# Kernel optimization log

Measured on AMD Instinct MI355X. Metric: run time of the kernel, lower is better.

## Reference

```python
import jax, jax.numpy as jnp
import numpy as np

TOKENS, IN_F, OUT_F = 65536, 1024, 1024


def setup_inputs() -> dict:
    key = jax.random.key(0)
    kx, kw = jax.random.split(key)
    x = jax.random.normal(kx, (TOKENS, IN_F), dtype=jnp.float32)
    weight = jax.random.normal(kw, (OUT_F, IN_F), dtype=jnp.float32) * 0.05
    return {"x": x, "weight": weight}


def reference(x, weight):
    # per-output-row scale: alpha = mean(|w|) over in_features
    alpha = jnp.mean(jnp.abs(weight), axis=1, keepdims=True)  # [out, 1]
    w_bin = jnp.sign(weight) * alpha                          # [out, in]
    # F.linear(x, w_bin) == x @ w_bin.T
    return jnp.einsum("ti,oi->to", x, w_bin)
```

## Files before the change

### kernel.cpp

```cpp
#include <hip/hip_runtime.h>


typedef _Float16 half8 __attribute__((ext_vector_type(8)));
typedef _Float16 half4v __attribute__((ext_vector_type(4)));
typedef float f32x4 __attribute__((ext_vector_type(4)));

#define TOKENS 65536
#define INF 1024
#define OUTF 1024
#define BM 256
#define BN 256
#define BK 32
#define NKT 32

__device__ __forceinline__ void gload_lds16(const void* g, void* l) {
  __builtin_amdgcn_global_load_lds(
      (const __attribute__((address_space(1))) unsigned int*)g,
      (__attribute__((address_space(3))) unsigned int*)l, 16, 0, 0);
}

__device__ __forceinline__ half8 cvt8(f32x4 a, f32x4 b) {
  half8 h;
  h[0] = (_Float16)a[0]; h[1] = (_Float16)a[1];
  h[2] = (_Float16)a[2]; h[3] = (_Float16)a[3];
  h[4] = (_Float16)b[0]; h[5] = (_Float16)b[1];
  h[6] = (_Float16)b[2]; h[7] = (_Float16)b[3];
  return h;
}

#define ALOAD(d0, d1, ap)                                                      \
  asm volatile("global_load_dwordx4 %0, %2, off\n\t"                           \
               "global_load_dwordx4 %1, %2, off offset:16"                     \
               : "=&v"(d0), "=&v"(d1)                                          \
               : "v"(ap)                                                       \
               : "memory")

__global__ __launch_bounds__(256) void bl_prep(const float* __restrict__ w,
                                               _Float16* __restrict__ sbin,
                                               float* __restrict__ alpha) {
  const int o = blockIdx.x;
  const int tid = threadIdx.x;
  const float4 v = ((const float4*)(w + (size_t)o * INF))[tid];
  float s = fabsf(v.x) + fabsf(v.y) + fabsf(v.z) + fabsf(v.w);
  half4v h;
  h[0] = (_Float16)((v.x > 0.f) ? 1.f : ((v.x < 0.f) ? -1.f : 0.f));
  h[1] = (_Float16)((v.y > 0.f) ? 1.f : ((v.y < 0.f) ? -1.f : 0.f));
  h[2] = (_Float16)((v.z > 0.f) ? 1.f : ((v.z < 0.f) ? -1.f : 0.f));
  h[3] = (_Float16)((v.w > 0.f) ? 1.f : ((v.w < 0.f) ? -1.f : 0.f));
  *(half4v*)(sbin + (size_t)o * INF + tid * 4) = h;
#pragma unroll
  for (int off = 32; off > 0; off >>= 1) s += __shfl_down(s, off, 64);
  __shared__ float red[4];
  const int wave = tid >> 6, lane = tid & 63;
  if (lane == 0) red[wave] = s;
  __syncthreads();
  if (tid == 0) alpha[o] = (red[0] + red[1] + red[2] + red[3]) * (1.0f / 1024.0f);
}

__global__ __launch_bounds__(512, 1) void bl_gemm(const float* __restrict__ x,
                                                  const _Float16* __restrict__ sbin,
                                                  const float* __restrict__ alpha,
                                                  float* __restrict__ out) {
  __shared__ _Float16 ldsA[4][BM * BK];
  __shared__ _Float16 ldsB[4][BN * BK];

  const int tid = threadIdx.x;
  const int lane = tid & 63;
  const int wid = tid >> 6;
  const int l15 = lane & 15;
  const int kc = lane >> 4;
  const int wr = wid >> 2;
  const int wc = wid & 3;

  const int bid = blockIdx.x;
  const int wgid = (bid & 7) * 128 + (bid >> 3);
  const int bm0 = (wgid >> 2) * BM;
  const int bn0 = (wgid & 3) * BN;

  const int rw = tid >> 2;
  const int cA = tid & 3;
  const int swz = cA ^ ((rw >> 1) & 3);

  size_t aOff[2], bOff[2];
  int aWr[2], bDst[2];
#pragma unroll
  for (int h = 0; h < 2; ++h) {
    aOff[h] = (size_t)(bm0 + h * 128 + rw) * INF + cA * 8;
    bOff[h] = (size_t)(bn0 + h * 128 + rw) * INF + swz * 8;
    aWr[h] = (h * 128 + rw) * 64 + swz * 16;
    bDst[h] = h * 8192 + tid * 16;
  }
  const int sl = (kc ^ ((l15 >> 1) & 3)) * 16;
  const int aRdB = (wr * 128 + l15) * 64 + sl;
  const int bRdB = (wc * 64 + l15) * 64 + sl;

  f32x4 acc[8][4] = {};
  f32x4 stA[2][2][2];
  half8 bf0, bf1, bf2, bf3;

  {
#pragma unroll
    for (int t = 0; t < 2; ++t)
#pragma unroll
      for (int h = 0; h < 2; ++h) {
        f32x4 v0 = *(const f32x4*)(x + aOff[h] + t * BK);
        f32x4 v1 = *(const f32x4*)(x + aOff[h] + t * BK + 4);
        *(half8*)((char*)&ldsA[t][0] + aWr[h]) = cvt8(v0, v1);
      }
#pragma unroll
    for (int t = 0; t < 2; ++t)
#pragma unroll
      for (int h = 0; h < 2; ++h)
        gload_lds16(sbin + bOff[h] + t * BK, (char*)&ldsB[t][0] + bDst[h]);
    ALOAD(stA[0][0][0], stA[0][0][1], x + aOff[0] + 2 * BK);
    ALOAD(stA[0][1][0], stA[0][1][1], x + aOff[1] + 2 * BK);
    ALOAD(stA[1][0][0], stA[1][0][1], x + aOff[0] + 3 * BK);
    ALOAD(stA[1][1][0], stA[1][1][1], x + aOff[1] + 3 * BK);
    asm volatile("s_waitcnt vmcnt(0) lgkmcnt(0)" ::: "memory");
    __builtin_amdgcn_s_barrier();
  }

#define PH(Tk_, KM_, H_)                                                       \
  {                                                                            \
    constexpr int bRd_ = (KM_) & 3;                                            \
    constexpr int bWr_ = ((KM_) + 2) & 3;                                      \
    constexpr int p_ = (KM_) & 1;                                              \
    const int tA_ = ((Tk_) + 4 < NKT) ? (Tk_) + 4 : NKT - 1;                   \
    const int tB_ = ((Tk_) + 2 < NKT) ? (Tk_) + 2 : NKT - 1;                   \
    asm volatile("s_waitcnt vmcnt(10)" ::: "memory");                          \
    __builtin_amdgcn_sched_barrier(0);                                         \
    *(half8*)((char*)&ldsA[bWr_][0] + aWr[H_]) =                               \
        cvt8(stA[p_][H_][0], stA[p_][H_][1]);                                  \
    ALOAD(stA[p_][H_][0], stA[p_][H_][1], x + aOff[H_] + tA_ * BK);            \
    gload_lds16(sbin + bOff[H_] + tB_ * BK, (char*)&ldsB[bWr_][0] + bDst[H_]); \
    if (H_) asm volatile("s_waitcnt vmcnt(6) lgkmcnt(0)" ::: "memory");        \
    half8 af0 = *(const half8*)((const char*)&ldsA[bRd_][0] + aRdB + ((H_)*4 + 0) * 1024); \
    half8 af1 = *(const half8*)((const char*)&ldsA[bRd_][0] + aRdB + ((H_)*4 + 1) * 1024); \
    half8 af2 = *(const half8*)((const char*)&ldsA[bRd_][0] + aRdB + ((H_)*4 + 2) * 1024); \
    half8 af3 = *(const half8*)((const char*)&ldsA[bRd_][0] + aRdB + ((H_)*4 + 3) * 1024); \
    if (!(H_)) {                                                               \
      bf0 = *(const half8*)((const char*)&ldsB[bRd_][0] + bRdB + 0);           \
      bf1 = *(const half8*)((const char*)&ldsB[bRd_][0] + bRdB + 1024);        \
      bf2 = *(const half8*)((const char*)&ldsB[bRd_][0] + bRdB + 2048);        \
      bf3 = *(const half8*)((const char*)&ldsB[bRd_][0] + bRdB + 3072);        \
    }                                                                          \
    __builtin_amdgcn_s_barrier();                                              \
    __builtin_amdgcn_s_setprio(1);                                             \
    acc[(H_)*4 + 0][0] = __builtin_amdgcn_mfma_f32_16x16x32_f16(af0, bf0, acc[(H_)*4 + 0][0], 0, 0, 0); \
    acc[(H_)*4 + 0][1] = __builtin_amdgcn_mfma_f32_16x16x32_f16(af0, bf1, acc[(H_)*4 + 0][1], 0, 0, 0); \
    acc[(H_)*4 + 0][2] = __builtin_amdgcn_mfma_f32_16x16x32_f16(af0, bf2, acc[(H_)*4 + 0][2], 0, 0, 0); \
    acc[(H_)*4 + 0][3] = __builtin_amdgcn_mfma_f32_16x16x32_f16(af0, bf3, acc[(H_)*4 + 0][3], 0, 0, 0); \
    acc[(H_)*4 + 1][0] = __builtin_amdgcn_mfma_f32_16x16x32_f16(af1, bf0, acc[(H_)*4 + 1][0], 0, 0, 0); \
    acc[(H_)*4 + 1][1] = __builtin_amdgcn_mfma_f32_16x16x32_f16(af1, bf1, acc[(H_)*4 + 1][1], 0, 0, 0); \
    acc[(H_)*4 + 1][2] = __builtin_amdgcn_mfma_f32_16x16x32_f16(af1, bf2, acc[(H_)*4 + 1][2], 0, 0, 0); \
    acc[(H_)*4 + 1][3] = __builtin_amdgcn_mfma_f32_16x16x32_f16(af1, bf3, acc[(H_)*4 + 1][3], 0, 0, 0); \
    acc[(H_)*4 + 2][0] = __builtin_amdgcn_mfma_f32_16x16x32_f16(af2, bf0, acc[(H_)*4 + 2][0], 0, 0, 0); \
    acc[(H_)*4 + 2][1] = __builtin_amdgcn_mfma_f32_16x16x32_f16(af2, bf1, acc[(H_)*4 + 2][1], 0, 0, 0); \
    acc[(H_)*4 + 2][2] = __builtin_amdgcn_mfma_f32_16x16x32_f16(af2, bf2, acc[(H_)*4 + 2][2], 0, 0, 0); \
    acc[(H_)*4 + 2][3] = __builtin_amdgcn_mfma_f32_16x16x32_f16(af2, bf3, acc[(H_)*4 + 2][3], 0, 0, 0); \
    acc[(H_)*4 + 3][0] = __builtin_amdgcn_mfma_f32_16x16x32_f16(af3, bf0, acc[(H_)*4 + 3][0], 0, 0, 0); \
    acc[(H_)*4 + 3][1] = __builtin_amdgcn_mfma_f32_16x16x32_f16(af3, bf1, acc[(H_)*4 + 3][1], 0, 0, 0); \
    acc[(H_)*4 + 3][2] = __builtin_amdgcn_mfma_f32_16x16x32_f16(af3, bf2, acc[(H_)*4 + 3][2], 0, 0, 0); \
    acc[(H_)*4 + 3][3] = __builtin_amdgcn_mfma_f32_16x16x32_f16(af3, bf3, acc[(H_)*4 + 3][3], 0, 0, 0); \
    __builtin_amdgcn_s_setprio(0);                                             \
    __builtin_amdgcn_s_barrier();                                              \
  }

#pragma unroll 1
  for (int tq = 0; tq < 8; ++tq) {
    const int TB = tq * 4;
    PH(TB + 0, 0, 0)
    PH(TB + 0, 0, 1)
    PH(TB + 1, 1, 0)
    PH(TB + 1, 1, 1)
    PH(TB + 2, 2, 0)
    PH(TB + 2, 2, 1)
    PH(TB + 3, 3, 0)
    PH(TB + 3, 3, 1)
  }
#undef PH

  float al[4];
#pragma unroll
  for (int n = 0; n < 4; ++n) al[n] = alpha[bn0 + wc * 64 + n * 16 + l15];
#pragma unroll
  for (int m = 0; m < 8; ++m) {
    const int row0 = bm0 + wr * 128 + m * 16 + kc * 4;
#pragma unroll
    for (int n = 0; n < 4; ++n) {
      const int col = bn0 + wc * 64 + n * 16 + l15;
#pragma unroll
      for (int j = 0; j < 4; ++j)
        out[(size_t)(row0 + j) * OUTF + col] = acc[m][n][j] * al[n];
    }
  }
}

extern "C" void kernel_launch(void* const* d_in, const int* in_sizes, int n_in,
                              void* d_out, int out_size, void* d_ws, size_t ws_size,
                              hipStream_t stream) {
  const float* x = (const float*)d_in[0];
  const float* w = (const float*)d_in[1];
  float* out = (float*)d_out;
  _Float16* sbin = (_Float16*)d_ws;
  float* alpha = (float*)((char*)d_ws + (size_t)OUTF * INF * 2);

  bl_prep<<<dim3(OUTF), dim3(256), 0, stream>>>(w, sbin, alpha);
  bl_gemm<<<dim3((TOKENS / BM) * (OUTF / BN)), dim3(512), 0, stream>>>(x, sbin, alpha, out);
}
```

Before: 214.4 us.

## Load A fragments directly into registers, drop A LDS staging, double-buffer B

Each wave now reads its x fragments straight from global memory into registers and converts them to fp16 just before the MFMAs, so x is no longer staged through LDS. Only the binarized weights go through a smaller, two-buffer LDS ring. The wave grid changes from 2x4 to 4x2, and launch bounds ask for two blocks per CU to raise occupancy. The trade-off is that the hand-tuned waitcnt/setprio pipeline is replaced by plain __syncthreads, and the x loads follow the MFMA fragment layout, so each lane reads 32 contiguous bytes rather than fully coalesced rows.

```diff
diff --git a/kernel.cpp b/kernel.cpp
--- a/kernel.cpp
+++ b/kernel.cpp
@@ -27,13 +27,6 @@
   h[6] = (_Float16)b[2]; h[7] = (_Float16)b[3];
   return h;
 }
-
-#define ALOAD(d0, d1, ap)                                                      \
-  asm volatile("global_load_dwordx4 %0, %2, off\n\t"                           \
-               "global_load_dwordx4 %1, %2, off offset:16"                     \
-               : "=&v"(d0), "=&v"(d1)                                          \
-               : "v"(ap)                                                       \
-               : "memory")
 
 __global__ __launch_bounds__(256) void bl_prep(const float* __restrict__ w,
                                                _Float16* __restrict__ sbin,
@@ -57,141 +50,147 @@
   if (tid == 0) alpha[o] = (red[0] + red[1] + red[2] + red[3]) * (1.0f / 1024.0f);
 }
 
-__global__ __launch_bounds__(512, 1) void bl_gemm(const float* __restrict__ x,
+__global__ __launch_bounds__(512, 2) void bl_gemm(const float* __restrict__ x,
                                                   const _Float16* __restrict__ sbin,
                                                   const float* __restrict__ alpha,
                                                   float* __restrict__ out) {
-  __shared__ _Float16 ldsA[4][BM * BK];
-  __shared__ _Float16 ldsB[4][BN * BK];
+  __shared__ _Float16 ldsB[2][BN * BK];
 
   const int tid = threadIdx.x;
   const int lane = tid & 63;
   const int wid = tid >> 6;
   const int l15 = lane & 15;
   const int kc = lane >> 4;
-  const int wr = wid >> 2;
-  const int wc = wid & 3;
+  const int wr = wid >> 1;
+  const int wc = wid & 1;
 
   const int bid = blockIdx.x;
   const int wgid = (bid & 7) * 128 + (bid >> 3);
   const int bm0 = (wgid >> 2) * BM;
   const int bn0 = (wgid & 3) * BN;
 
-  const int rw = tid >> 2;
-  const int cA = tid & 3;
-  const int swz = cA ^ ((rw >> 1) & 3);
-
-  size_t aOff[2], bOff[2];
-  int aWr[2], bDst[2];
-#pragma unroll
-  for (int h = 0; h < 2; ++h) {
-    aOff[h] = (size_t)(bm0 + h * 128 + rw) * INF + cA * 8;
-    bOff[h] = (size_t)(bn0 + h * 128 + rw) * INF + swz * 8;
-    aWr[h] = (h * 128 + rw) * 64 + swz * 16;
-    bDst[h] = h * 8192 + tid * 16;
-  }
-  const int sl = (kc ^ ((l15 >> 1) & 3)) * 16;
-  const int aRdB = (wr * 128 + l15) * 64 + sl;
-  const int bRdB = (wc * 64 + l15) * 64 + sl;
-
-  f32x4 acc[8][4] = {};
-  f32x4 stA[2][2][2];
-  half8 bf0, bf1, bf2, bf3;
-
-  {
-#pragma unroll
-    for (int t = 0; t < 2; ++t)
-#pragma unroll
-      for (int h = 0; h < 2; ++h) {
-        f32x4 v0 = *(const f32x4*)(x + aOff[h] + t * BK);
-        f32x4 v1 = *(const f32x4*)(x + aOff[h] + t * BK + 4);
-        *(half8*)((char*)&ldsA[t][0] + aWr[h]) = cvt8(v0, v1);
+  size_t bSrc[2];
+  int bDst[2];
+#pragma unroll
+  for (int p = 0; p < 2; ++p) {
+    const int ci = p * 512 + tid;
+    const int row = ci >> 2;
+    const int c = (ci & 3) ^ ((row >> 1) & 3);
+    bSrc[p] = (size_t)(bn0 + row) * INF + c * 8;
+    bDst[p] = ci * 16;
+  }
+  int bRd[8];
+#pragma unroll
+  for (int nf = 0; nf < 8; ++nf) {
+    const int row = wc * 128 + nf * 16 + l15;
+    bRd[nf] = row * 64 + ((kc ^ ((row >> 1) & 3)) << 4);
+  }
+  const float* aBase = x + (size_t)(bm0 + wr * 64 + l15) * INF + kc * 8;
+
+  f32x4 acc[4][8] = {};
+  f32x4 a0[4][2], a1[4][2];
+
+#define LOADA(dst_, ko_)                                                       \
+  {                                                                            \
+    _Pragma("unroll") for (int mf = 0; mf < 4; ++mf) {                         \
+      dst_[mf][0] = *(const f32x4*)(aBase + mf * 16384 + (ko_));               \
+      dst_[mf][1] = *(const f32x4*)(aBase + mf * 16384 + (ko_) + 4);           \
+    }                                                                          \
+  }
+
+#define STAGEB(buf_, tk_)                                                      \
+  {                                                                            \
+    gload_lds16(sbin + bSrc[0] + (size_t)(tk_)*BK, (char*)&ldsB[buf_][0] + bDst[0]); \
+    gload_lds16(sbin + bSrc[1] + (size_t)(tk_)*BK, (char*)&ldsB[buf_][0] + bDst[1]); \
+  }
+
+#define COMPUTE(buf_, areg_)                                                   \
+  {                                                                            \
+    half8 af0 = cvt8(areg_[0][0], areg_[0][1]);                                \
+    half8 af1 = cvt8(areg_[1][0], areg_[1][1]);                                \
+    half8 af2 = cvt8(areg_[2][0], areg_[2][1]);                                \
+    half8 af3 = cvt8(areg_[3][0], areg_[3][1]);                                \
+    const char* pb_ = (const char*)&ldsB[buf_][0];                             \
+    half8 b0 = *(const half8*)(pb_ + bRd[0]);                                  \
+    half8 b1 = *(const half8*)(pb_ + bRd[1]);                                  \
+    half8 b2 = *(const half8*)(pb_ + bRd[2]);                                  \
+    half8 b3 = *(const half8*)(pb_ + bRd[3]);                                  \
+    acc[0][0] = __builtin_amdgcn_mfma_f32_16x16x32_f16(af0, b0, acc[0][0], 0, 0, 0); \
+    acc[1][0] = __builtin_amdgcn_mfma_f32_16x16x32_f16(af1, b0, acc[1][0], 0, 0, 0); \
+    acc[2][0] = __builtin_amdgcn_mfma_f32_16x16x32_f16(af2, b0, acc[2][0], 0, 0, 0); \
+    acc[3][0] = __builtin_amdgcn_mfma_f32_16x16x32_f16(af3, b0, acc[3][0], 0, 0, 0); \
+    acc[0][1] = __builtin_amdgcn_mfma_f32_16x16x32_f16(af0, b1, acc[0][1], 0, 0, 0); \
+    acc[1][1] = __builtin_amdgcn_mfma_f32_16x16x32_f16(af1, b1, acc[1][1], 0, 0, 0); \
+    acc[2][1] = __builtin_amdgcn_mfma_f32_16x16x32_f16(af2, b1, acc[2][1], 0, 0, 0); \
+    acc[3][1] = __builtin_amdgcn_mfma_f32_16x16x32_f16(af3, b1, acc[3][1], 0, 0, 0); \
+    acc[0][2] = __builtin_amdgcn_mfma_f32_16x16x32_f16(af0, b2, acc[0][2], 0, 0, 0); \
+    acc[1][2] = __builtin_amdgcn_mfma_f32_16x16x32_f16(af1, b2, acc[1][2], 0, 0, 0); \
+    acc[2][2] = __builtin_amdgcn_mfma_f32_16x16x32_f16(af2, b2, acc[2][2], 0, 0, 0); \
+    acc[3][2] = __builtin_amdgcn_mfma_f32_16x16x32_f16(af3, b2, acc[3][2], 0, 0, 0); \
+    acc[0][3] = __builtin_amdgcn_mfma_f32_16x16x32_f16(af0, b3, acc[0][3], 0, 0, 0); \
+    acc[1][3] = __builtin_amdgcn_mfma_f32_16x16x32_f16(af1, b3, acc[1][3], 0, 0, 0); \
+    acc[2][3] = __builtin_amdgcn_mfma_f32_16x16x32_f16(af2, b3, acc[2][3], 0, 0, 0); \
+    acc[3][3] = __builtin_amdgcn_mfma_f32_16x16x32_f16(af3, b3, acc[3][3], 0, 0, 0); \
+    b0 = *(const half8*)(pb_ + bRd[4]);                                        \
+    b1 = *(const half8*)(pb_ + bRd[5]);                                        \
+    b2 = *(const half8*)(pb_ + bRd[6]);                                        \
+    b3 = *(const half8*)(pb_ + bRd[7]);                                        \
+    acc[0][4] = __builtin_amdgcn_mfma_f32_16x16x32_f16(af0, b0, acc[0][4], 0, 0, 0); \
+    acc[1][4] = __builtin_amdgcn_mfma_f32_16x16x32_f16(af1, b0, acc[1][4], 0, 0, 0); \
+    acc[2][4] = __builtin_amdgcn_mfma_f32_16x16x32_f16(af2, b0, acc[2][4], 0, 0, 0); \
+    acc[3][4] = __builtin_amdgcn_mfma_f32_16x16x32_f16(af3, b0, acc[3][4], 0, 0, 0); \
+    acc[0][5] = __builtin_amdgcn_mfma_f32_16x16x32_f16(af0, b1, acc[0][5], 0, 0, 0); \
+    acc[1][5] = __builtin_amdgcn_mfma_f32_16x16x32_f16(af1, b1, acc[1][5], 0, 0, 0); \
+    acc[2][5] = __builtin_amdgcn_mfma_f32_16x16x32_f16(af2, b1, acc[2][5], 0, 0, 0); \
+    acc[3][5] = __builtin_amdgcn_mfma_f32_16x16x32_f16(af3, b1, acc[3][5], 0, 0, 0); \
+    acc[0][6] = __builtin_amdgcn_mfma_f32_16x16x32_f16(af0, b2, acc[0][6], 0, 0, 0); \
+    acc[1][6] = __builtin_amdgcn_mfma_f32_16x16x32_f16(af1, b2, acc[1][6], 0, 0, 0); \
+    acc[2][6] = __builtin_amdgcn_mfma_f32_16x16x32_f16(af2, b2, acc[2][6], 0, 0, 0); \
+    acc[3][6] = __builtin_amdgcn_mfma_f32_16x16x32_f16(af3, b2, acc[3][6], 0, 0, 0); \
+    acc[0][7] = __builtin_amdgcn_mfma_f32_16x16x32_f16(af0, b3, acc[0][7], 0, 0, 0); \
+    acc[1][7] = __builtin_amdgcn_mfma_f32_16x16x32_f16(af1, b3, acc[1][7], 0, 0, 0); \
+    acc[2][7] = __builtin_amdgcn_mfma_f32_16x16x32_f16(af2, b3, acc[2][7], 0, 0, 0); \
+    acc[3][7] = __builtin_amdgcn_mfma_f32_16x16x32_f16(af3, b3, acc[3][7], 0, 0, 0); \
+  }
+
+  STAGEB(0, 0);
+  LOADA(a0, 0);
+  __syncthreads();
+
+#pragma unroll 1
+  for (int u = 0; u < NKT / 2; ++u) {
+    const int Te = 2 * u;
+    {
+      STAGEB(1, Te + 1);
+      LOADA(a1, (size_t)(Te + 1) * BK);
+      COMPUTE(0, a0);
+      __syncthreads();
+    }
+    {
+      if (Te + 2 < NKT) {
+        STAGEB(0, Te + 2);
+        LOADA(a0, (size_t)(Te + 2) * BK);
       }
-#pragma unroll
-    for (int t = 0; t < 2; ++t)
-#pragma unroll
-      for (int h = 0; h < 2; ++h)
-        gload_lds16(sbin + bOff[h] + t * BK, (char*)&ldsB[t][0] + bDst[h]);
-    ALOAD(stA[0][0][0], stA[0][0][1], x + aOff[0] + 2 * BK);
-    ALOAD(stA[0][1][0], stA[0][1][1], x + aOff[1] + 2 * BK);
-    ALOAD(stA[1][0][0], stA[1][0][1], x + aOff[0] + 3 * BK);
-    ALOAD(stA[1][1][0], stA[1][1][1], x + aOff[1] + 3 * BK);
-    asm volatile("s_waitcnt vmcnt(0) lgkmcnt(0)" ::: "memory");
-    __builtin_amdgcn_s_barrier();
-  }
-
-#define PH(Tk_, KM_, H_)                                                       \
-  {                                                                            \
-    constexpr int bRd_ = (KM_) & 3;                                            \
-    constexpr int bWr_ = ((KM_) + 2) & 3;                                      \
-    constexpr int p_ = (KM_) & 1;                                              \
-    const int tA_ = ((Tk_) + 4 < NKT) ? (Tk_) + 4 : NKT - 1;                   \
-    const int tB_ = ((Tk_) + 2 < NKT) ? (Tk_) + 2 : NKT - 1;                   \
-    asm volatile("s_waitcnt vmcnt(10)" ::: "memory");                          \
-    __builtin_amdgcn_sched_barrier(0);                                         \
-    *(half8*)((char*)&ldsA[bWr_][0] + aWr[H_]) =                               \
-        cvt8(stA[p_][H_][0], stA[p_][H_][1]);                                  \
-    ALOAD(stA[p_][H_][0], stA[p_][H_][1], x + aOff[H_] + tA_ * BK);            \
-    gload_lds16(sbin + bOff[H_] + tB_ * BK, (char*)&ldsB[bWr_][0] + bDst[H_]); \
-    if (H_) asm volatile("s_waitcnt vmcnt(6) lgkmcnt(0)" ::: "memory");        \
-    half8 af0 = *(const half8*)((const char*)&ldsA[bRd_][0] + aRdB + ((H_)*4 + 0) * 1024); \
-    half8 af1 = *(const half8*)((const char*)&ldsA[bRd_][0] + aRdB + ((H_)*4 + 1) * 1024); \
-    half8 af2 = *(const half8*)((const char*)&ldsA[bRd_][0] + aRdB + ((H_)*4 + 2) * 1024); \
-    half8 af3 = *(const half8*)((const char*)&ldsA[bRd_][0] + aRdB + ((H_)*4 + 3) * 1024); \
-    if (!(H_)) {                                                               \
-      bf0 = *(const half8*)((const char*)&ldsB[bRd_][0] + bRdB + 0);           \
-      bf1 = *(const half8*)((const char*)&ldsB[bRd_][0] + bRdB + 1024);        \
-      bf2 = *(const half8*)((const char*)&ldsB[bRd_][0] + bRdB + 2048);        \
-      bf3 = *(const half8*)((const char*)&ldsB[bRd_][0] + bRdB + 3072);        \
-    }                                                                          \
-    __builtin_amdgcn_s_barrier();                                              \
-    __builtin_amdgcn_s_setprio(1);                                             \
-    acc[(H_)*4 + 0][0] = __builtin_amdgcn_mfma_f32_16x16x32_f16(af0, bf0, acc[(H_)*4 + 0][0], 0, 0, 0); \
-    acc[(H_)*4 + 0][1] = __builtin_amdgcn_mfma_f32_16x16x32_f16(af0, bf1, acc[(H_)*4 + 0][1], 0, 0, 0); \
-    acc[(H_)*4 + 0][2] = __builtin_amdgcn_mfma_f32_16x16x32_f16(af0, bf2, acc[(H_)*4 + 0][2], 0, 0, 0); \
-    acc[(H_)*4 + 0][3] = __builtin_amdgcn_mfma_f32_16x16x32_f16(af0, bf3, acc[(H_)*4 + 0][3], 0, 0, 0); \
-    acc[(H_)*4 + 1][0] = __builtin_amdgcn_mfma_f32_16x16x32_f16(af1, bf0, acc[(H_)*4 + 1][0], 0, 0, 0); \
-    acc[(H_)*4 + 1][1] = __builtin_amdgcn_mfma_f32_16x16x32_f16(af1, bf1, acc[(H_)*4 + 1][1], 0, 0, 0); \
-    acc[(H_)*4 + 1][2] = __builtin_amdgcn_mfma_f32_16x16x32_f16(af1, bf2, acc[(H_)*4 + 1][2], 0, 0, 0); \
-    acc[(H_)*4 + 1][3] = __builtin_amdgcn_mfma_f32_16x16x32_f16(af1, bf3, acc[(H_)*4 + 1][3], 0, 0, 0); \
-    acc[(H_)*4 + 2][0] = __builtin_amdgcn_mfma_f32_16x16x32_f16(af2, bf0, acc[(H_)*4 + 2][0], 0, 0, 0); \
-    acc[(H_)*4 + 2][1] = __builtin_amdgcn_mfma_f32_16x16x32_f16(af2, bf1, acc[(H_)*4 + 2][1], 0, 0, 0); \
-    acc[(H_)*4 + 2][2] = __builtin_amdgcn_mfma_f32_16x16x32_f16(af2, bf2, acc[(H_)*4 + 2][2], 0, 0, 0); \
-    acc[(H_)*4 + 2][3] = __builtin_amdgcn_mfma_f32_16x16x32_f16(af2, bf3, acc[(H_)*4 + 2][3], 0, 0, 0); \
-    acc[(H_)*4 + 3][0] = __builtin_amdgcn_mfma_f32_16x16x32_f16(af3, bf0, acc[(H_)*4 + 3][0], 0, 0, 0); \
-    acc[(H_)*4 + 3][1] = __builtin_amdgcn_mfma_f32_16x16x32_f16(af3, bf1, acc[(H_)*4 + 3][1], 0, 0, 0); \
-    acc[(H_)*4 + 3][2] = __builtin_amdgcn_mfma_f32_16x16x32_f16(af3, bf2, acc[(H_)*4 + 3][2], 0, 0, 0); \
-    acc[(H_)*4 + 3][3] = __builtin_amdgcn_mfma_f32_16x16x32_f16(af3, bf3, acc[(H_)*4 + 3][3], 0, 0, 0); \
-    __builtin_amdgcn_s_setprio(0);                                             \
-    __builtin_amdgcn_s_barrier();                                              \
-  }
-
-#pragma unroll 1
-  for (int tq = 0; tq < 8; ++tq) {
-    const int TB = tq * 4;
-    PH(TB + 0, 0, 0)
-    PH(TB + 0, 0, 1)
-    PH(TB + 1, 1, 0)
-    PH(TB + 1, 1, 1)
-    PH(TB + 2, 2, 0)
-    PH(TB + 2, 2, 1)
-    PH(TB + 3, 3, 0)
-    PH(TB + 3, 3, 1)
-  }
-#undef PH
-
-  float al[4];
-#pragma unroll
-  for (int n = 0; n < 4; ++n) al[n] = alpha[bn0 + wc * 64 + n * 16 + l15];
-#pragma unroll
-  for (int m = 0; m < 8; ++m) {
-    const int row0 = bm0 + wr * 128 + m * 16 + kc * 4;
-#pragma unroll
-    for (int n = 0; n < 4; ++n) {
-      const int col = bn0 + wc * 64 + n * 16 + l15;
+      COMPUTE(1, a1);
+      __syncthreads();
+    }
+  }
+#undef COMPUTE
+#undef STAGEB
+#undef LOADA
+
+  float al[8];
+#pragma unroll
+  for (int n = 0; n < 8; ++n) al[n] = alpha[bn0 + wc * 128 + n * 16 + l15];
+#pragma unroll
+  for (int mf = 0; mf < 4; ++mf) {
+    const int row0 = bm0 + wr * 64 + mf * 16 + kc * 4;
+#pragma unroll
+    for (int n = 0; n < 8; ++n) {
+      const int col = bn0 + wc * 128 + n * 16 + l15;
 #pragma unroll
       for (int j = 0; j < 4; ++j)
-        out[(size_t)(row0 + j) * OUTF + col] = acc[m][n][j] * al[n];
+        out[(size_t)(row0 + j) * OUTF + col] = acc[mf][n][j] * al[n];
     }
   }
 }
```

New measurement: 408.5 us. 1.9x slower.
